# Performance work log

Measured on AMD Instinct MI355X. Metric: run time of the kernel, lower is better.

## Reference

```python
import jax, jax.numpy as jnp
import numpy as np
import math

N = 50000      # nodes
E = 800000     # edges
F_IN = 64      # input node features
H = 4          # heads
C = 32         # hidden_channels (per-head dim)
HC = H * C     # 128
ED = 4         # edge_dim
G = 1000       # graphs in batch


def _lin(key, fin, fout, bias=True):
    k1, k2 = jax.random.split(key)
    w = jax.random.normal(k1, (fin, fout), jnp.float32) * (1.0 / math.sqrt(fin))
    if bias:
        b = jax.random.normal(k2, (fout,), jnp.float32) * 0.02
        return w, b
    return w


def setup_inputs() -> dict:
    key = jax.random.key(0)
    ks = jax.random.split(key, 24)
    x = jax.random.normal(ks[0], (N, F_IN), jnp.float32)
    edge_index = jax.random.randint(ks[1], (2, E), 0, N)
    edge_attr = jax.random.normal(ks[2], (E, ED), jnp.float32)
    batch = jnp.sort(jax.random.randint(ks[3], (N,), 0, G))
    inp = {"x": x, "edge_index": edge_index, "edge_attr": edge_attr, "batch": batch}
    fins = [F_IN, HC, HC]
    i = 4
    for l in range(3):
        fin = fins[l]
        inp[f"wq{l+1}"], inp[f"bq{l+1}"] = _lin(ks[i], fin, HC); i += 1
        inp[f"wk{l+1}"], inp[f"bk{l+1}"] = _lin(ks[i], fin, HC); i += 1
        inp[f"wv{l+1}"], inp[f"bv{l+1}"] = _lin(ks[i], fin, HC); i += 1
        inp[f"we{l+1}"] = _lin(ks[i], ED, HC, bias=False); i += 1
        inp[f"ws{l+1}"], inp[f"bs{l+1}"] = _lin(ks[i], fin, HC); i += 1
    inp["wlin"], inp["blin"] = _lin(ks[i], HC, 1)
    return inp


def _segment_softmax(alpha, seg, n):
    # numerically-stable softmax over edges grouped by destination node
    m = jax.ops.segment_max(alpha, seg, num_segments=n)
    m = jnp.where(jnp.isfinite(m), m, 0.0)
    a = jnp.exp(alpha - m[seg])
    s = jax.ops.segment_sum(a, seg, num_segments=n)
    return a / (s[seg] + 1e-16)


def _conv(x, src, dst, ea, wq, bq, wk, bk, wv, bv, we, ws, bs):
    # PyG TransformerConv (concat=True, root_weight=True, beta=False)
    n = x.shape[0]
    q = (x @ wq + bq).reshape(n, H, C)
    k = (x @ wk + bk).reshape(n, H, C)
    v = (x @ wv + bv).reshape(n, H, C)
    e = (ea @ we).reshape(-1, H, C)          # [E,H,C] edge projection
    kj = k[src] + e                           # key of source + edge
    alpha = jnp.einsum('ehc,ehc->eh', q[dst], kj) / math.sqrt(C)  # [E,H]
    alpha = _segment_softmax(alpha, dst, n)
    msg = (v[src] + e) * alpha[..., None]     # [E,H,C]
    out = jax.ops.segment_sum(msg, dst, num_segments=n).reshape(n, HC)
    return out + x @ ws + bs                  # skip connection


def reference(x, edge_index, edge_attr, batch,
              wq1, bq1, wk1, bk1, wv1, bv1, we1, ws1, bs1,
              wq2, bq2, wk2, bk2, wv2, bv2, we2, ws2, bs2,
              wq3, bq3, wk3, bk3, wv3, bv3, we3, ws3, bs3,
              wlin, blin):
    src, dst = edge_index[0], edge_index[1]
    h = jax.nn.relu(_conv(x, src, dst, edge_attr, wq1, bq1, wk1, bk1, wv1, bv1, we1, ws1, bs1))
    h = jax.nn.relu(_conv(h, src, dst, edge_attr, wq2, bq2, wk2, bk2, wv2, bv2, we2, ws2, bs2))
    h = _conv(h, src, dst, edge_attr, wq3, bq3, wk3, bk3, wv3, bv3, we3, ws3, bs3)
    # global_mean_pool
    s = jax.ops.segment_sum(h, batch, num_segments=G)
    cnt = jax.ops.segment_sum(jnp.ones((h.shape[0],), h.dtype), batch, num_segments=G)
    pooled = s / jnp.maximum(cnt, 1.0)[:, None]
    # dropout is identity in eval mode
    return pooled @ wlin + blin
```

## Files before the change

### kernel.cpp

```cpp
#include <hip/hip_runtime.h>
#include <math.h>

#define NN 50000
#define EE 800000
#define GG 1000

typedef __attribute__((ext_vector_type(2))) _Float16 h2f;
typedef __attribute__((ext_vector_type(4))) _Float16 h4f;
typedef __attribute__((ext_vector_type(8))) _Float16 h8f;
typedef __attribute__((ext_vector_type(4))) float f32x4;

#if __has_builtin(__builtin_amdgcn_fdot2)
#define FDOT2(a, b, c) __builtin_amdgcn_fdot2((a), (b), (c), false)
#else
#define FDOT2(a, b, c) ((float)(a)[0] * (float)(b)[0] + (float)(a)[1] * (float)(b)[1] + (c))
#endif

static inline int ceil_div(int a, int b) { return (a + b - 1) / b; }

union EU { int2 i; h4f h; };


__global__ __launch_bounds__(256) void hist_k(const int* __restrict__ ei, int* __restrict__ cnt)
{
    int e = blockIdx.x * 256 + threadIdx.x;
    if (e >= EE) return;
    atomicAdd(&cnt[ei[EE + e]], 1);
}

__global__ __launch_bounds__(1024) void scan1_k(const int* __restrict__ cnt, int n,
                                                int* __restrict__ rowptr, int* __restrict__ bsum,
                                                const int* __restrict__ batch,
                                                int* __restrict__ gptr)
{
    __shared__ int tmp[1024];
    const int tid = threadIdx.x;
    const int i = blockIdx.x * 1024 + tid;
    tmp[tid] = (i < n) ? cnt[i] : 0;
    __syncthreads();
    for (int off = 1; off < 1024; off <<= 1) {
        int t = (tid >= off) ? tmp[tid - off] : 0;
        __syncthreads();
        tmp[tid] += t;
        __syncthreads();
    }
    if (i < n) rowptr[i + 1] = tmp[tid];
    if (tid == 1023) bsum[blockIdx.x] = tmp[1023];
    if (i < NN) {
        int b = batch[i];
        int bp = (i == 0) ? -1 : batch[i - 1];
        for (int g = bp + 1; g <= b; ++g) gptr[g] = i;
        if (i == NN - 1) for (int g = b + 1; g <= GG; ++g) gptr[g] = NN;
    }
}

__global__ __launch_bounds__(1024) void scan3_k(int* __restrict__ rowptr,
                                                int* __restrict__ wcur,
                                                const int* __restrict__ bsum, int n)
{
    __shared__ int base_s;
    const int tid = threadIdx.x;
    if (tid < 64) {
        int v = (tid < (int)blockIdx.x) ? bsum[tid] : 0;
#pragma unroll
        for (int off = 1; off < 64; off <<= 1) v += __shfl_xor(v, off);
        if (tid == 0) base_s = v;
    }
    __syncthreads();
    const int base = base_s;
    int i = blockIdx.x * 1024 + tid;
    if (i < n) {
        int v = rowptr[i + 1] + base;
        rowptr[i + 1] = v;
        if (i + 1 < n) wcur[i + 1] = v;
    }
    if (i == 0) { rowptr[0] = 0; wcur[0] = 0; }
}

__global__ __launch_bounds__(256) void scatter_k(const int* __restrict__ ei,
                                                 const float4* __restrict__ ea,
                                                 int* __restrict__ wcur,
                                                 int4* __restrict__ edges)
{
    int e = blockIdx.x * 256 + threadIdx.x;
    if (e >= EE) return;
    int dst = ei[EE + e];
    int pos = atomicAdd(&wcur[dst], 1);
    float4 a = ea[e];
    EU u; u.h = h4f{(_Float16)a.x, (_Float16)a.y, (_Float16)a.z, (_Float16)a.w};
    edges[pos] = make_int4(ei[e], u.i.x, u.i.y, 0);
}

struct W12 { const float* w[12]; };

__global__ __launch_bounds__(64) void shuffle_w12(W12 ws, _Float16* __restrict__ out)
{
    const int m = blockIdx.y;
    const int K = (m < 4) ? 64 : 128;
    const int nblk = (K / 16) * 8;
    if (blockIdx.x >= nblk) return;
    const int s = blockIdx.x >> 3, c16 = blockIdx.x & 7;
    const int lane = threadIdx.x;
    const float* __restrict__ w = ws.w[m];
    const int kbase = s * 16 + (lane >> 4) * 4;
    const int col = c16 * 16 + (lane & 15);
    h4f h;
#pragma unroll
    for (int j = 0; j < 4; ++j) h[j] = (_Float16)w[(size_t)(kbase + j) * 128 + col];
    size_t base = (m < 4) ? (size_t)m * 64 * 128
                          : (size_t)4 * 64 * 128 + (size_t)(m - 4) * 128 * 128;
    reinterpret_cast<h4f*>(out + base)[(size_t)blockIdx.x * 64 + lane] = h;
}

template<int K, bool F32IN>
__global__ __launch_bounds__(256) void gemm_mfma(
    const void* __restrict__ xin, const _Float16* __restrict__ wshuf,
    const float* __restrict__ bq, const float* __restrict__ bk,
    const float* __restrict__ bv, const float* __restrict__ bs,
    _Float16* __restrict__ qout, _Float16* __restrict__ kout,
    _Float16* __restrict__ vout, _Float16* __restrict__ skout)
{
    constexpr int KS = K / 16;
    constexpr int PADK = K + 8;
    __shared__ _Float16 xs[64 * PADK];
    __shared__ _Float16 wt[K * 128];
    const int t = threadIdx.x;
    const int bn = blockIdx.x * 64;
    const int m = blockIdx.y;

    if (F32IN) {
        const float* xf = (const float*)xin;
        constexpr int C4 = K / 4;
        for (int idx = t; idx < 64 * C4; idx += 256) {
            const int row = idx / C4, c4 = idx % C4;
            float4 val = make_float4(0.f, 0.f, 0.f, 0.f);
            if (bn + row < NN)
                val = reinterpret_cast<const float4*>(xf)[(size_t)(bn + row) * C4 + c4];
            h4f h = {(_Float16)val.x, (_Float16)val.y, (_Float16)val.z, (_Float16)val.w};
            *reinterpret_cast<h4f*>(&xs[row * PADK + c4 * 4]) = h;
        }
    } else {
        const _Float16* xh = (const _Float16*)xin;
        constexpr int CH = K / 8;
        for (int idx = t; idx < 64 * CH; idx += 256) {
            const int row = idx / CH, ch = idx % CH;
            h8f val = {0, 0, 0, 0, 0, 0, 0, 0};
            if (bn + row < NN)
                val = reinterpret_cast<const h8f*>(xh + (size_t)(bn + row) * K)[ch];
            *reinterpret_cast<h8f*>(&xs[row * PADK + ch * 8]) = val;
        }
    }
    {
        const h8f* __restrict__ wg = reinterpret_cast<const h8f*>(wshuf + (size_t)m * K * 128);
        h8f* __restrict__ wl8 = reinterpret_cast<h8f*>(wt);
        constexpr int WH8 = K * 16;
        for (int idx = t; idx < WH8; idx += 256) wl8[idx] = wg[idx];
    }
    __syncthreads();

    const int wid = t >> 6, lane = t & 63;
    const int rloc = wid * 16 + (lane & 15);
    const int ko = (lane >> 4) * 4;
    h4f b[KS];
#pragma unroll
    for (int s = 0; s < KS; ++s)
        b[s] = *reinterpret_cast<const h4f*>(&xs[rloc * PADK + s * 16 + ko]);

    const int node = bn + rloc;
    const int hcq = (lane >> 4) * 4;
    const float* bias[4] = {bq, bk, bv, bs};
    _Float16* outs[4] = {qout, kout, vout, skout};
    const h4f* __restrict__ wl = reinterpret_cast<const h4f*>(wt);

    f32x4 acc[8];
#pragma unroll
    for (int c = 0; c < 8; ++c) acc[c] = {0, 0, 0, 0};
#pragma unroll
    for (int c = 0; c < 8; ++c)
#pragma unroll
        for (int s = 0; s < KS; ++s) {
            h4f af = wl[(s * 8 + c) * 64 + lane];
            acc[c] = __builtin_amdgcn_mfma_f32_16x16x16f16(af, b[s], acc[c], 0, 0, 0);
        }
    if (node < NN) {
        const float* bm = bias[m];
        _Float16* dst = outs[m];
#pragma unroll
        for (int c = 0; c < 8; ++c) {
            const int hc = c * 16 + hcq;
            const float4 bb = *reinterpret_cast<const float4*>(&bm[hc]);
            h4f oh = {(_Float16)(acc[c][0] + bb.x), (_Float16)(acc[c][1] + bb.y),
                      (_Float16)(acc[c][2] + bb.z), (_Float16)(acc[c][3] + bb.w)};
            *reinterpret_cast<h4f*>(&dst[(size_t)node * 128 + hc]) = oh;
        }
    }
}

__global__ __launch_bounds__(256, 8) void node_agg(
    const int* __restrict__ rowptr, const int4* __restrict__ edges,
    const _Float16* __restrict__ qh, const _Float16* __restrict__ kh,
    const _Float16* __restrict__ vh, const float* __restrict__ we,
    const _Float16* __restrict__ sk, _Float16* __restrict__ houth, int relu)
{
    __shared__ float we_s[4 * 128];
    const int t = threadIdx.x;
    if (t < 128)
        reinterpret_cast<float4*>(we_s)[t] = reinterpret_cast<const float4*>(we)[t];
    __syncthreads();
    const int node = blockIdx.x * 8 + (t >> 5);
    if (node >= NN) return;
    const int lane32 = t & 31;
    const int g = lane32 >> 4;
    const int sub = lane32 & 15, ch0 = sub * 8;
    const int beg = rowptr[node], end = rowptr[node + 1];
    const int deg = end - beg;

    const float sc = 0.17677669529663687f * 1.4426950408889634f;
    const h8f q8 = *reinterpret_cast<const h8f*>(&qh[(size_t)node * 128 + ch0]);
    float qf[8];
#pragma unroll
    for (int j = 0; j < 8; ++j) qf[j] = (float)q8[j] * sc;
    h2f qp[4];
#pragma unroll
    for (int i = 0; i < 4; ++i) {
        qp[i][0] = (_Float16)qf[2 * i];
        qp[i][1] = (_Float16)qf[2 * i + 1];
    }

    float qe[4];
#pragma unroll
    for (int d = 0; d < 4; ++d) {
        const float4 wa = *reinterpret_cast<const float4*>(&we_s[d * 128 + ch0]);
        const float4 wb = *reinterpret_cast<const float4*>(&we_s[d * 128 + ch0 + 4]);
        float pq = wa.x * qf[0] + wa.y * qf[1] + wa.z * qf[2] + wa.w * qf[3]
                 + wb.x * qf[4] + wb.y * qf[5] + wb.z * qf[6] + wb.w * qf[7];
        pq += __shfl_xor(pq, 1); pq += __shfl_xor(pq, 2);
        qe[d] = pq;
    }

    float m = -1e30f, s = 0.f;
    float acc[8] = {0, 0, 0, 0, 0, 0, 0, 0};
    float T[4] = {0, 0, 0, 0};

    const int nt = (deg + 1) >> 1;
    int p = beg + g;
    for (int i = 0; i < nt; ++i, p += 2) {
        const bool act = p < end;
        const int4 r = edges[act ? p : beg];
        const int4 ki = *reinterpret_cast<const int4*>(&kh[(size_t)r.x * 128 + ch0]);
        const int4 vi = *reinterpret_cast<const int4*>(&vh[(size_t)r.x * 128 + ch0]);
        float al = FDOT2(qp[0], __builtin_bit_cast(h2f, ki.x), 0.0f);
        al = FDOT2(qp[1], __builtin_bit_cast(h2f, ki.y), al);
        al = FDOT2(qp[2], __builtin_bit_cast(h2f, ki.z), al);
        al = FDOT2(qp[3], __builtin_bit_cast(h2f, ki.w), al);
        al += __shfl_xor(al, 1); al += __shfl_xor(al, 2);
        const h2f e01 = __builtin_bit_cast(h2f, r.y);
        const h2f e23 = __builtin_bit_cast(h2f, r.z);
        const float f0 = (float)e01[0], f1 = (float)e01[1];
        const float f2 = (float)e23[0], f3 = (float)e23[1];
        al += f0 * qe[0] + f1 * qe[1] + f2 * qe[2] + f3 * qe[3];
        al = act ? al : -1e30f;
        if (__any(al > m + 10.0f)) {
            const float mn = fmaxf(m, al);
            const float rr = exp2f(m - mn);
            s *= rr;
#pragma unroll
            for (int j = 0; j < 8; ++j) acc[j] *= rr;
#pragma unroll
            for (int d = 0; d < 4; ++d) T[d] *= rr;
            m = mn;
        }
        const float pe = exp2f(al - m);
        s += pe;
        const h2f v01 = __builtin_bit_cast(h2f, vi.x);
        const h2f v23 = __builtin_bit_cast(h2f, vi.y);
        const h2f v45 = __builtin_bit_cast(h2f, vi.z);
        const h2f v67 = __builtin_bit_cast(h2f, vi.w);
        acc[0] += pe * (float)v01[0]; acc[1] += pe * (float)v01[1];
        acc[2] += pe * (float)v23[0]; acc[3] += pe * (float)v23[1];
        acc[4] += pe * (float)v45[0]; acc[5] += pe * (float)v45[1];
        acc[6] += pe * (float)v67[0]; acc[7] += pe * (float)v67[1];
        T[0] += pe * f0; T[1] += pe * f1; T[2] += pe * f2; T[3] += pe * f3;
    }

    {
        const float mo = __shfl_xor(m, 16);
        const float so = __shfl_xor(s, 16);
        const float mn = fmaxf(m, mo);
        const float r1 = exp2f(m - mn), r2 = exp2f(mo - mn);
        s = s * r1 + so * r2;
#pragma unroll
        for (int j = 0; j < 8; ++j) {
            const float ao = __shfl_xor(acc[j], 16);
            acc[j] = acc[j] * r1 + ao * r2;
        }
#pragma unroll
        for (int d = 0; d < 4; ++d) {
            const float To = __shfl_xor(T[d], 16);
            T[d] = T[d] * r1 + To * r2;
        }
        m = mn;
    }

    if (g == 0) {
        const float inv = 1.0f / (s + 1e-16f);
        float4 wa[4], wb[4];
#pragma unroll
        for (int d = 0; d < 4; ++d) {
            wa[d] = *reinterpret_cast<const float4*>(&we_s[d * 128 + ch0]);
            wb[d] = *reinterpret_cast<const float4*>(&we_s[d * 128 + ch0 + 4]);
        }
        const h8f sk8 = *reinterpret_cast<const h8f*>(&sk[(size_t)node * 128 + ch0]);
        float ov[8];
        ov[0] = (acc[0] + wa[0].x * T[0] + wa[1].x * T[1] + wa[2].x * T[2] + wa[3].x * T[3]) * inv + (float)sk8[0];
        ov[1] = (acc[1] + wa[0].y * T[0] + wa[1].y * T[1] + wa[2].y * T[2] + wa[3].y * T[3]) * inv + (float)sk8[1];
        ov[2] = (acc[2] + wa[0].z * T[0] + wa[1].z * T[1] + wa[2].z * T[2] + wa[3].z * T[3]) * inv + (float)sk8[2];
        ov[3] = (acc[3] + wa[0].w * T[0] + wa[1].w * T[1] + wa[2].w * T[2] + wa[3].w * T[3]) * inv + (float)sk8[3];
        ov[4] = (acc[4] + wb[0].x * T[0] + wb[1].x * T[1] + wb[2].x * T[2] + wb[3].x * T[3]) * inv + (float)sk8[4];
        ov[5] = (acc[5] + wb[0].y * T[0] + wb[1].y * T[1] + wb[2].y * T[2] + wb[3].y * T[3]) * inv + (float)sk8[5];
        ov[6] = (acc[6] + wb[0].z * T[0] + wb[1].z * T[1] + wb[2].z * T[2] + wb[3].z * T[3]) * inv + (float)sk8[6];
        ov[7] = (acc[7] + wb[0].w * T[0] + wb[1].w * T[1] + wb[2].w * T[2] + wb[3].w * T[3]) * inv + (float)sk8[7];
        h8f oh;
#pragma unroll
        for (int j = 0; j < 8; ++j) {
            float v = relu ? fmaxf(ov[j], 0.f) : ov[j];
            oh[j] = (_Float16)v;
        }
        *reinterpret_cast<h8f*>(&houth[(size_t)node * 128 + ch0]) = oh;
    }
}


__global__ __launch_bounds__(128) void head_k(
    const _Float16* __restrict__ h, const int* __restrict__ gptr,
    const float* __restrict__ wlin, const float* __restrict__ blin,
    float* __restrict__ out)
{
    __shared__ float red[128];
    const int g = blockIdx.x;
    const int t = threadIdx.x;
    const int beg = gptr[g], end = gptr[g + 1];
    float p = 0.f;
    for (int n = beg; n < end; ++n) p += (float)h[(size_t)n * 128 + t];
    p *= wlin[t];
    red[t] = p;
    __syncthreads();
    for (int off = 64; off; off >>= 1) {
        if (t < off) red[t] += red[t + off];
        __syncthreads();
    }
    if (t == 0) out[g] = red[0] / fmaxf((float)(end - beg), 1.0f) + blin[0];
}

extern "C" void kernel_launch(void* const* d_in, const int* in_sizes, int n_in,
                              void* d_out, int out_size, void* d_ws, size_t ws_size,
                              hipStream_t stream)
{
    const float* x     = (const float*)d_in[0];
    const int*   ei    = (const int*)d_in[1];
    const float* ea    = (const float*)d_in[2];
    const int*   batch = (const int*)d_in[3];
    auto W = [&](int i) { return (const float*)d_in[i]; };

    char* wsb = (char*)d_ws;
    size_t off = 0;
    auto alloc = [&](size_t bytes) { void* p = wsb + off; off += (bytes + 15) & ~15ull; return p; };

    int4*  edges    = (int4*)alloc((size_t)EE * 16);
    _Float16* qh    = (_Float16*)alloc((size_t)NN * 128 * 2);
    _Float16* kh    = (_Float16*)alloc((size_t)NN * 128 * 2);
    _Float16* vh    = (_Float16*)alloc((size_t)NN * 128 * 2);
    _Float16* sk    = (_Float16*)alloc((size_t)NN * 128 * 2);
    _Float16* hh    = (_Float16*)alloc((size_t)NN * 128 * 2);
    _Float16* wshuf = (_Float16*)alloc(((size_t)4 * 64 * 128 + 8 * 128 * 128) * 2);
    int* cnt    = (int*)alloc((size_t)NN * 4);
    int* rowptr = (int*)alloc((size_t)(NN + 1) * 4);
    int* wcur   = (int*)alloc((size_t)NN * 4);
    int* gptr   = (int*)alloc((size_t)(GG + 1) * 4);
    int* bsum   = (int*)alloc((size_t)64 * 4);

    hipMemsetAsync(cnt, 0, NN * sizeof(int), stream);
    hist_k<<<ceil_div(EE, 256), 256, 0, stream>>>(ei, cnt);
    const int NB = ceil_div(NN, 1024);
    scan1_k<<<NB, 1024, 0, stream>>>(cnt, NN, rowptr, bsum, batch, gptr);
    scan3_k<<<NB, 1024, 0, stream>>>(rowptr, wcur, bsum, NN);
    scatter_k<<<ceil_div(EE, 256), 256, 0, stream>>>(ei, (const float4*)ea, wcur, edges);

    W12 w12 = {{ W(4), W(6), W(8), W(11),
                 W(13), W(15), W(17), W(20),
                 W(22), W(24), W(26), W(29) }};
    shuffle_w12<<<dim3(64, 12), 64, 0, stream>>>(w12, wshuf);
    const size_t wsz1 = (size_t)4 * 64 * 128;
    const size_t wsz2 = (size_t)4 * 128 * 128;

    auto layer = [&](int K, const void* xin, const _Float16* wsh, int relu, int wb) {
        dim3 gg(ceil_div(NN, 64), 4);
        if (K == 64)
            gemm_mfma<64, true><<<gg, 256, 0, stream>>>(
                xin, wsh, W(wb + 1), W(wb + 3), W(wb + 5), W(wb + 8), qh, kh, vh, sk);
        else
            gemm_mfma<128, false><<<gg, 256, 0, stream>>>(
                xin, wsh, W(wb + 1), W(wb + 3), W(wb + 5), W(wb + 8), qh, kh, vh, sk);
        node_agg<<<ceil_div(NN, 8), 256, 0, stream>>>(
            rowptr, edges, qh, kh, vh, W(wb + 6), sk, hh, relu);
    };

    layer(64,  x,  wshuf, 1, 4);
    layer(128, hh, wshuf + wsz1, 1, 13);
    layer(128, hh, wshuf + wsz1 + wsz2, 0, 22);

    head_k<<<GG, 128, 0, stream>>>(hh, gptr, W(31), W(32), (float*)d_out);
}
```

Baseline: 423.0 us.

## Interleave K and V per node and split GEMM output columns across blocks

K and V projections are now written into one interleaved buffer of 256 halves per node, so the edge gather in node aggregation reads both from the same 512-byte region of a source row. The GEMM grid doubles along y, and each block computes half of the 128 output columns, which halves the weight tile in shared memory and the accumulator registers. The cost is that each block reloads the input X tile, doubling X reads, in exchange for higher occupancy and better gather locality.

New measurement: 426.3 us. About the same (+0.8%).

```diff
diff --git a/kernel.cpp b/kernel.cpp
--- a/kernel.cpp
+++ b/kernel.cpp
@@ -117,16 +117,18 @@
     const void* __restrict__ xin, const _Float16* __restrict__ wshuf,
     const float* __restrict__ bq, const float* __restrict__ bk,
     const float* __restrict__ bv, const float* __restrict__ bs,
-    _Float16* __restrict__ qout, _Float16* __restrict__ kout,
-    _Float16* __restrict__ vout, _Float16* __restrict__ skout)
+    _Float16* __restrict__ qout, _Float16* __restrict__ kvout,
+    _Float16* __restrict__ skout)
 {
     constexpr int KS = K / 16;
     constexpr int PADK = K + 8;
     __shared__ _Float16 xs[64 * PADK];
-    __shared__ _Float16 wt[K * 128];
+    __shared__ _Float16 wt[K * 64];
     const int t = threadIdx.x;
     const int bn = blockIdx.x * 64;
-    const int m = blockIdx.y;
+    const int m = blockIdx.y >> 1;
+    const int chalf = blockIdx.y & 1;
+    const int c0 = chalf * 4;
 
     if (F32IN) {
         const float* xf = (const float*)xin;
@@ -153,8 +155,12 @@
     {
         const h8f* __restrict__ wg = reinterpret_cast<const h8f*>(wshuf + (size_t)m * K * 128);
         h8f* __restrict__ wl8 = reinterpret_cast<h8f*>(wt);
-        constexpr int WH8 = K * 16;
-        for (int idx = t; idx < WH8; idx += 256) wl8[idx] = wg[idx];
+        constexpr int NH8 = KS * 4 * 32;
+        for (int j = t; j < NH8; j += 256) {
+            const int s = j >> 7, rem = j & 127;
+            const int cc = rem >> 5, l2 = rem & 31;
+            wl8[(s * 4 + cc) * 32 + l2] = wg[(s * 8 + c0 + cc) * 32 + l2];
+        }
     }
     __syncthreads();
 
@@ -169,38 +175,41 @@
     const int node = bn + rloc;
     const int hcq = (lane >> 4) * 4;
     const float* bias[4] = {bq, bk, bv, bs};
-    _Float16* outs[4] = {qout, kout, vout, skout};
     const h4f* __restrict__ wl = reinterpret_cast<const h4f*>(wt);
 
-    f32x4 acc[8];
-#pragma unroll
-    for (int c = 0; c < 8; ++c) acc[c] = {0, 0, 0, 0};
-#pragma unroll
-    for (int c = 0; c < 8; ++c)
+    f32x4 acc[4];
+#pragma unroll
+    for (int cc = 0; cc < 4; ++cc) acc[cc] = {0, 0, 0, 0};
+#pragma unroll
+    for (int cc = 0; cc < 4; ++cc)
 #pragma unroll
         for (int s = 0; s < KS; ++s) {
-            h4f af = wl[(s * 8 + c) * 64 + lane];
-            acc[c] = __builtin_amdgcn_mfma_f32_16x16x16f16(af, b[s], acc[c], 0, 0, 0);
+            h4f af = wl[(s * 4 + cc) * 64 + lane];
+            acc[cc] = __builtin_amdgcn_mfma_f32_16x16x16f16(af, b[s], acc[cc], 0, 0, 0);
         }
     if (node < NN) {
         const float* bm = bias[m];
-        _Float16* dst = outs[m];
-#pragma unroll
-        for (int c = 0; c < 8; ++c) {
-            const int hc = c * 16 + hcq;
+#pragma unroll
+        for (int cc = 0; cc < 4; ++cc) {
+            const int hc = (c0 + cc) * 16 + hcq;
             const float4 bb = *reinterpret_cast<const float4*>(&bm[hc]);
-            h4f oh = {(_Float16)(acc[c][0] + bb.x), (_Float16)(acc[c][1] + bb.y),
-                      (_Float16)(acc[c][2] + bb.z), (_Float16)(acc[c][3] + bb.w)};
-            *reinterpret_cast<h4f*>(&dst[(size_t)node * 128 + hc]) = oh;
+            h4f oh = {(_Float16)(acc[cc][0] + bb.x), (_Float16)(acc[cc][1] + bb.y),
+                      (_Float16)(acc[cc][2] + bb.z), (_Float16)(acc[cc][3] + bb.w)};
+            _Float16* dst;
+            if (m == 0)      dst = &qout[(size_t)node * 128 + hc];
+            else if (m == 1) dst = &kvout[(size_t)node * 256 + hc];
+            else if (m == 2) dst = &kvout[(size_t)node * 256 + 128 + hc];
+            else             dst = &skout[(size_t)node * 128 + hc];
+            *reinterpret_cast<h4f*>(dst) = oh;
         }
     }
 }
 
 __global__ __launch_bounds__(256, 8) void node_agg(
     const int* __restrict__ rowptr, const int4* __restrict__ edges,
-    const _Float16* __restrict__ qh, const _Float16* __restrict__ kh,
-    const _Float16* __restrict__ vh, const float* __restrict__ we,
-    const _Float16* __restrict__ sk, _Float16* __restrict__ houth, int relu)
+    const _Float16* __restrict__ qh, const _Float16* __restrict__ kv,
+    const float* __restrict__ we, const _Float16* __restrict__ sk,
+    _Float16* __restrict__ houth, int relu)
 {
     __shared__ float we_s[4 * 128];
     const int t = threadIdx.x;
@@ -247,8 +256,9 @@
     for (int i = 0; i < nt; ++i, p += 2) {
         const bool act = p < end;
         const int4 r = edges[act ? p : beg];
-        const int4 ki = *reinterpret_cast<const int4*>(&kh[(size_t)r.x * 128 + ch0]);
-        const int4 vi = *reinterpret_cast<const int4*>(&vh[(size_t)r.x * 128 + ch0]);
+        const size_t kvbase = (size_t)r.x * 256 + ch0;
+        const int4 ki = *reinterpret_cast<const int4*>(&kv[kvbase]);
+        const int4 vi = *reinterpret_cast<const int4*>(&kv[kvbase + 128]);
         float al = FDOT2(qp[0], __builtin_bit_cast(h2f, ki.x), 0.0f);
         al = FDOT2(qp[1], __builtin_bit_cast(h2f, ki.y), al);
         al = FDOT2(qp[2], __builtin_bit_cast(h2f, ki.z), al);
@@ -368,8 +378,7 @@
 
     int4*  edges    = (int4*)alloc((size_t)EE * 16);
     _Float16* qh    = (_Float16*)alloc((size_t)NN * 128 * 2);
-    _Float16* kh    = (_Float16*)alloc((size_t)NN * 128 * 2);
-    _Float16* vh    = (_Float16*)alloc((size_t)NN * 128 * 2);
+    _Float16* kv    = (_Float16*)alloc((size_t)NN * 256 * 2);
     _Float16* sk    = (_Float16*)alloc((size_t)NN * 128 * 2);
     _Float16* hh    = (_Float16*)alloc((size_t)NN * 128 * 2);
     _Float16* wshuf = (_Float16*)alloc(((size_t)4 * 64 * 128 + 8 * 128 * 128) * 2);
@@ -394,15 +403,15 @@
     const size_t wsz2 = (size_t)4 * 128 * 128;
 
     auto layer = [&](int K, const void* xin, const _Float16* wsh, int relu, int wb) {
-        dim3 gg(ceil_div(NN, 64), 4);
+        dim3 gg(ceil_div(NN, 64), 8);
         if (K == 64)
             gemm_mfma<64, true><<<gg, 256, 0, stream>>>(
-                xin, wsh, W(wb + 1), W(wb + 3), W(wb + 5), W(wb + 8), qh, kh, vh, sk);
+                xin, wsh, W(wb + 1), W(wb + 3), W(wb + 5), W(wb + 8), qh, kv, sk);
         else
             gemm_mfma<128, false><<<gg, 256, 0, stream>>>(
-                xin, wsh, W(wb + 1), W(wb + 3), W(wb + 5), W(wb + 8), qh, kh, vh, sk);
+                xin, wsh, W(wb + 1), W(wb + 3), W(wb + 5), W(wb + 8), qh, kv, sk);
         node_agg<<<ceil_div(NN, 8), 256, 0, stream>>>(
-            rowptr, edges, qh, kh, vh, W(wb + 6), sk, hh, relu);
+            rowptr, edges, qh, kv, W(wb + 6), sk, hh, relu);
     };
 
     layer(64,  x,  wshuf, 1, 4);
```
